# Kernel optimization log

Hardware: AMD Instinct MI355X
Metric: run time of the kernel (lower is better)

## Reference

```python
import jax, jax.numpy as jnp
import numpy as np

TOP_K = 2
NUM_EXPERTS = 8

def setup_inputs() -> dict:
    key = jax.random.key(0)
    k_x, k_r, k_g, k_u, k_d = jax.random.split(key, 5)
    B, L, D, H, E = 1, 2048, 1024, 2048, NUM_EXPERTS
    scale = 0.02  # keep router logits / activations in a sane range
    return {
        "x": jax.random.normal(k_x, (B, L, D), dtype=jnp.float32),
        "router_w": jax.random.normal(k_r, (D, E), dtype=jnp.float32) * scale,
        "gate_w": jax.random.normal(k_g, (E, D, H), dtype=jnp.float32) * scale,
        "up_w": jax.random.normal(k_u, (E, D, H), dtype=jnp.float32) * scale,
        "down_w": jax.random.normal(k_d, (E, H, D), dtype=jnp.float32) * scale,
    }

def reference(x, router_w, gate_w, up_w, down_w):
    # x: (B, L, D)
    B, L, D = x.shape
    T = B * L
    E = router_w.shape[1]
    xf = x.reshape(T, D)

    # --- router: top-k softmax over selected logits (Mixtral-style) ---
    logits = xf @ router_w                      # (T, E)
    top_vals, top_idx = jax.lax.top_k(logits, TOP_K)  # (T, K)
    top_w = jax.nn.softmax(top_vals, axis=-1)   # (T, K)

    # combine weights scattered to dense (T, E); zeros for unrouted experts
    combine = jnp.zeros((T, E), dtype=x.dtype).at[
        jnp.arange(T)[:, None], top_idx
    ].add(top_w)

    # --- experts: SwiGLU, computed per expert, zero-weight tokens masked by combine ---
    gate = jnp.einsum('td,edh->eth', xf, gate_w)   # (E, T, H)
    up = jnp.einsum('td,edh->eth', xf, up_w)       # (E, T, H)
    hidden = jax.nn.silu(gate) * up                # (E, T, H)
    expert_out = jnp.einsum('eth,ehd->etd', hidden, down_w)  # (E, T, D)

    # --- weighted combine (equivalent to scatter_add over sorted assignments) ---
    y = jnp.einsum('etd,te->td', expert_out, combine)  # (T, D)
    return y.reshape(B, L, D)
```

## Files before the change

kernel.cpp:

```cpp
#include <hip/hip_runtime.h>
#include <hip/hip_bf16.h>
#include <stdint.h>

#define T_TOK 2048
#define DIM   1024
#define HDIM  2048
#define NE    8
#define ROWS_PAD 4224
#define TSLOTS 40

typedef __attribute__((ext_vector_type(8))) short bf16x8;
typedef __attribute__((ext_vector_type(8))) unsigned short u16x8;
typedef __attribute__((ext_vector_type(4))) float f32x4;
typedef __attribute__((ext_vector_type(4))) unsigned int u32x4;

__device__ __forceinline__ unsigned short f2bf(float f) {
    union { __hip_bfloat16 h; unsigned short u; } cv;
    cv.h = __float2bfloat16(f);
    return cv.u;
}
__device__ __forceinline__ unsigned int f2bf2(float lo, float hi) {
    union { __hip_bfloat162 h; unsigned int u; } cv;
    cv.h = __float22bfloat162_rn(make_float2(lo, hi));
    return cv.u;
}
__device__ __forceinline__ float bf2f(unsigned short b) {
    union { unsigned int u; float f; } v; v.u = ((unsigned int)b) << 16;
    return v.f;
}

__device__ __forceinline__ void gload16(const void* g, void* l) {
    __builtin_amdgcn_global_load_lds(
        (const __attribute__((address_space(1))) void*)g,
        (__attribute__((address_space(3))) void*)l, 16, 0, 0);
}

__global__ void router_kernel(const float* __restrict__ x, const float* __restrict__ rw,
                              int* __restrict__ counts, int* __restrict__ top_idx,
                              float* __restrict__ top_w) {
    int wid = (blockIdx.x * blockDim.x + threadIdx.x) >> 6;
    int lane = threadIdx.x & 63;
    if (wid >= T_TOK) return;
    float acc[NE];
#pragma unroll
    for (int e = 0; e < NE; ++e) acc[e] = 0.f;
    const float* xr = x + (size_t)wid * DIM;
    for (int i = lane; i < DIM; i += 64) {
        float xv = xr[i];
        const float* wr = rw + (size_t)i * NE;
#pragma unroll
        for (int e = 0; e < NE; ++e) acc[e] += xv * wr[e];
    }
#pragma unroll
    for (int off = 32; off; off >>= 1) {
#pragma unroll
        for (int e = 0; e < NE; ++e) acc[e] += __shfl_xor(acc[e], off, 64);
    }
    if (lane == 0) {
        float v0 = -1e30f, v1 = -1e30f; int i0 = 0, i1 = 0;
#pragma unroll
        for (int e = 0; e < NE; ++e) {
            float v = acc[e];
            if (v > v0) { v1 = v0; i1 = i0; v0 = v; i0 = e; }
            else if (v > v1) { v1 = v; i1 = e; }
        }
        float e1 = __expf(v1 - v0);
        float s = 1.f + e1;
        top_idx[wid * 2]     = i0;
        top_idx[wid * 2 + 1] = i1;
        top_w[wid * 2]     = 1.f / s;
        top_w[wid * 2 + 1] = e1 / s;
        atomicAdd(&counts[i0], 1);
        atomicAdd(&counts[i1], 1);
    }
}

__global__ void scan_kernel(const int* __restrict__ counts, int* __restrict__ offsets,
                            int* __restrict__ cursors,
                            int* __restrict__ tl_e, int* __restrict__ tl_m) {
    if (threadIdx.x == 0) {
        int run = 0;
        for (int e = 0; e < NE; ++e) { offsets[e] = run; cursors[e] = run; run += counts[e]; }
        int n = 0;
        for (int e = 0; e < NE; ++e) {
            int mt = (counts[e] + 127) >> 7;
            for (int m = 0; m < mt && n < 64; ++m) { tl_e[n] = e; tl_m[n] = m; ++n; }
        }
        for (; n < 64; ++n) tl_e[n] = -1;
    }
}

__global__ void gather_kernel(const float* __restrict__ x, const int* __restrict__ top_idx,
                              const float* __restrict__ top_w, int* __restrict__ cursors,
                              int* __restrict__ row_tok, float* __restrict__ row_w,
                              unsigned short* __restrict__ Abuf) {
    int t = blockIdx.x;
    __shared__ int pos[2];
    if (threadIdx.x < 2) {
        int k = threadIdx.x;
        int e = top_idx[t * 2 + k];
        int p = atomicAdd(&cursors[e], 1);
        pos[k] = p;
        row_tok[p] = t;
        row_w[p] = top_w[t * 2 + k];
    }
    __syncthreads();
    const float4* xr = (const float4*)(x + (size_t)t * DIM);
    float4 v = xr[threadIdx.x];
    unsigned int lo = f2bf2(v.x, v.y), hi = f2bf2(v.z, v.w);
    uint2 b; b.x = lo; b.y = hi;
    uint2* A4 = (uint2*)Abuf;
    A4[(size_t)pos[0] * (DIM / 4) + threadIdx.x] = b;
    A4[(size_t)pos[1] * (DIM / 4) + threadIdx.x] = b;
}

__global__ __launch_bounds__(256, 2)
void gemm1_kernel(const unsigned short* __restrict__ Abuf,
                  const float* __restrict__ gw,
                  const float* __restrict__ uw,
                  unsigned short* __restrict__ Hbuf,
                  const int* __restrict__ offsets, const int* __restrict__ counts,
                  const int* __restrict__ tl_e, const int* __restrict__ tl_m) {
    const int slot = blockIdx.y;
    const int e = tl_e[slot];
    if (e < 0) return;
    const int mtile = tl_m[slot];
    const int cnt = counts[e];
    const int n0 = blockIdx.x * 64;
    const int row0 = offsets[e] + mtile * 128;

    __shared__ __align__(16) unsigned char lds_raw[65536];
    unsigned short* AsB = (unsigned short*)lds_raw;
    unsigned short* BgB = (unsigned short*)(lds_raw + 32768);
    unsigned short* BuB = (unsigned short*)(lds_raw + 49152);
    unsigned short* ex  = (unsigned short*)lds_raw;

    const int tid = threadIdx.x;
    const int lane = tid & 63;
    const int wave = tid >> 6;
    const int wm = wave >> 1;
    const int wu = wave & 1;

    f32x4 acc[4][4];
#pragma unroll
    for (int i = 0; i < 4; ++i)
#pragma unroll
        for (int j = 0; j < 4; ++j) acc[i][j] = (f32x4){0.f, 0.f, 0.f, 0.f};

    const int srow = tid >> 3;
    const int sc0 = tid & 7;
    const unsigned short* Aab = Abuf + (size_t)row0 * DIM;

    auto stageA = [&](int buf, int kt) {
#pragma unroll
        for (int i = 0; i < 4; ++i) {
            int row = i * 32 + srow;
            int csrc = sc0 ^ (row & 7);
            gload16(Aab + (size_t)row * DIM + kt + csrc * 8,
                    AsB + buf * 8192 + (i * 256 + tid) * 8);
        }
    };

    const int bn = tid & 63;
    const int bc0 = tid >> 6;
    const float* Bgb = gw + (size_t)e * DIM * HDIM + n0 + bn;
    const float* Bub = uw + (size_t)e * DIM * HDIM + n0 + bn;

    float bgl[2][8], bul[2][8];
    auto bload = [&](int kt) {
#pragma unroll
        for (int cc = 0; cc < 2; ++cc) {
            int c = bc0 + cc * 4;
            const float* gs = Bgb + (size_t)(kt + c * 8) * HDIM;
            const float* us = Bub + (size_t)(kt + c * 8) * HDIM;
#pragma unroll
            for (int jj = 0; jj < 8; ++jj) {
                bgl[cc][jj] = gs[(size_t)jj * HDIM];
                bul[cc][jj] = us[(size_t)jj * HDIM];
            }
        }
    };
    auto bwrite = [&](int buf) {
#pragma unroll
        for (int cc = 0; cc < 2; ++cc) {
            int c = bc0 + cc * 4;
            int la = bn * 64 + ((c ^ (bn & 7)) * 8);
            u32x4 vg, vu;
#pragma unroll
            for (int p = 0; p < 4; ++p) {
                vg[p] = f2bf2(bgl[cc][2 * p], bgl[cc][2 * p + 1]);
                vu[p] = f2bf2(bul[cc][2 * p], bul[cc][2 * p + 1]);
            }
            *(u32x4*)&BgB[buf * 4096 + la] = vg;
            *(u32x4*)&BuB[buf * 4096 + la] = vu;
        }
    };

    const int rsel = lane & 15;
    const int csrcf = lane >> 4;

    stageA(0, 0);
    bload(0);
    bwrite(0);
    int cur = 0;
    for (int kt = 0; kt < DIM; kt += 64) {
        __syncthreads();
        const bool pre = (kt + 64 < DIM);
        if (pre) { stageA(cur ^ 1, kt + 64); bload(kt + 64); }
        const unsigned short* Ac = AsB + cur * 8192;
        const unsigned short* Bc = (wu ? BuB : BgB) + cur * 4096;
#pragma unroll
        for (int kk = 0; kk < 2; ++kk) {
            bf16x8 af[4], bb[4];
#pragma unroll
            for (int i = 0; i < 4; ++i) {
                int ra = wm * 64 + i * 16 + rsel;
                af[i] = *(const bf16x8*)&Ac[ra * 64 + ((kk * 4 + csrcf) ^ (ra & 7)) * 8];
                int rb = i * 16 + rsel;
                bb[i] = *(const bf16x8*)&Bc[rb * 64 + ((kk * 4 + csrcf) ^ (rb & 7)) * 8];
            }
#pragma unroll
            for (int i = 0; i < 4; ++i)
#pragma unroll
                for (int j = 0; j < 4; ++j)
                    acc[i][j] = __builtin_amdgcn_mfma_f32_16x16x32_bf16(af[i], bb[j], acc[i][j], 0, 0, 0);
        }
        if (pre) bwrite(cur ^ 1);
        cur ^= 1;
    }

    const int c = lane & 15, rbase = (lane >> 4) * 4;
    const int obase = offsets[e];
    __syncthreads();
    if (wu) {
#pragma unroll
        for (int i = 0; i < 4; ++i)
#pragma unroll
            for (int r = 0; r < 4; ++r) {
                int row64 = i * 16 + rbase + r;
#pragma unroll
                for (int j = 0; j < 4; ++j)
                    ex[wm * 4096 + row64 * 64 + j * 16 + c] = f2bf(acc[i][j][r]);
            }
    }
    __syncthreads();
    if (!wu) {
#pragma unroll
        for (int i = 0; i < 4; ++i) {
#pragma unroll
            for (int r = 0; r < 4; ++r) {
                int row64 = i * 16 + rbase + r;
                int lrow = mtile * 128 + wm * 64 + row64;
                if (lrow < cnt) {
                    size_t orow = (size_t)(obase + lrow);
#pragma unroll
                    for (int j = 0; j < 4; ++j) {
                        float g = acc[i][j][r];
                        float u = bf2f(ex[wm * 4096 + row64 * 64 + j * 16 + c]);
                        float h = g * u / (1.f + __expf(-g));
                        Hbuf[orow * HDIM + n0 + j * 16 + c] = f2bf(h);
                    }
                }
            }
        }
    }
}

__global__ __launch_bounds__(256, 2)
void gemm2_kernel(const unsigned short* __restrict__ Hbuf,
                  const float* __restrict__ dw,
                  float* __restrict__ y,
                  const int* __restrict__ offsets, const int* __restrict__ counts,
                  const int* __restrict__ row_tok, const float* __restrict__ row_w,
                  const int* __restrict__ tl_e, const int* __restrict__ tl_m) {
    const int slot = blockIdx.y;
    const int e = tl_e[slot];
    if (e < 0) return;
    const int mtile = tl_m[slot];
    const int kc = blockIdx.z;
    const int cnt = counts[e];
    const int n0 = blockIdx.x * 128;
    const int row0 = offsets[e] + mtile * 128;

    __shared__ unsigned short As[2][128 * 64];
    __shared__ unsigned short Bs[2][128 * 64];

    const int tid = threadIdx.x;
    const int lane = tid & 63;
    const int wave = tid >> 6;
    const int wm = wave >> 1, wn = wave & 1;

    f32x4 acc[4][4];
#pragma unroll
    for (int i = 0; i < 4; ++i)
#pragma unroll
        for (int j = 0; j < 4; ++j) acc[i][j] = (f32x4){0.f, 0.f, 0.f, 0.f};

    const int srow0 = tid >> 3;
    const int sc0 = tid & 7;
    const unsigned short* Aab = Hbuf + (size_t)row0 * HDIM;

    auto stageA = [&](int buf, int kt) {
#pragma unroll
        for (int i = 0; i < 4; ++i) {
            int row = i * 32 + srow0;
            int csrc = sc0 ^ (row & 7);
            gload16(Aab + (size_t)row * HDIM + kt + csrc * 8,
                    &As[buf][(i * 256 + tid) * 8]);
        }
    };

    const int bn = tid & 127;
    const int bc0 = (tid >> 7) * 4;
    const float* Bbb = dw + (size_t)e * HDIM * DIM + n0 + bn;

    float bl[4][8];
    auto bload = [&](int kt) {
#pragma unroll
        for (int cc = 0; cc < 4; ++cc) {
            const float* bs = Bbb + (size_t)(kt + (bc0 + cc) * 8) * DIM;
#pragma unroll
            for (int jj = 0; jj < 8; ++jj)
                bl[cc][jj] = bs[(size_t)jj * DIM];
        }
    };
    auto bwrite = [&](int buf) {
#pragma unroll
        for (int cc = 0; cc < 4; ++cc) {
            int c = bc0 + cc;
            int la = bn * 64 + ((c ^ (bn & 7)) * 8);
            u32x4 v;
#pragma unroll
            for (int p = 0; p < 4; ++p)
                v[p] = f2bf2(bl[cc][2 * p], bl[cc][2 * p + 1]);
            *(u32x4*)&Bs[buf][la] = v;
        }
    };

    const int rsel = lane & 15;
    const int csrcf = lane >> 4;

    const int kbeg = kc * (HDIM / 2);
    const int kend = kbeg + (HDIM / 2);

    stageA(0, kbeg);
    bload(kbeg);
    bwrite(0);
    int cur = 0;
    for (int kt = kbeg; kt < kend; kt += 64) {
        __syncthreads();
        const bool pre = (kt + 64 < kend);
        if (pre) { stageA(cur ^ 1, kt + 64); bload(kt + 64); }
        const unsigned short* Ac = As[cur];
        const unsigned short* Bc = Bs[cur];
#pragma unroll
        for (int kk = 0; kk < 2; ++kk) {
            bf16x8 af[4], bf[4];
#pragma unroll
            for (int i = 0; i < 4; ++i) {
                int ra = wm * 64 + i * 16 + rsel;
                af[i] = *(const bf16x8*)&Ac[ra * 64 + ((kk * 4 + csrcf) ^ (ra & 7)) * 8];
                int rb = wn * 64 + i * 16 + rsel;
                bf[i] = *(const bf16x8*)&Bc[rb * 64 + ((kk * 4 + csrcf) ^ (rb & 7)) * 8];
            }
#pragma unroll
            for (int i = 0; i < 4; ++i)
#pragma unroll
                for (int j = 0; j < 4; ++j)
                    acc[i][j] = __builtin_amdgcn_mfma_f32_16x16x32_bf16(af[i], bf[j], acc[i][j], 0, 0, 0);
        }
        if (pre) bwrite(cur ^ 1);
        cur ^= 1;
    }

    const int c = lane & 15, rbase = (lane >> 4) * 4;
    const int obase = offsets[e];
#pragma unroll
    for (int i = 0; i < 4; ++i) {
#pragma unroll
        for (int r = 0; r < 4; ++r) {
            int lrow = mtile * 128 + wm * 64 + i * 16 + rbase + r;
            if (lrow < cnt) {
                int grow = obase + lrow;
                int tok = row_tok[grow];
                float w = row_w[grow];
#pragma unroll
                for (int j = 0; j < 4; ++j) {
                    atomicAdd(&y[(size_t)tok * DIM + n0 + wn * 64 + j * 16 + c], w * acc[i][j][r]);
                }
            }
        }
    }
}

extern "C" void kernel_launch(void* const* d_in, const int* in_sizes, int n_in,
                              void* d_out, int out_size, void* d_ws, size_t ws_size,
                              hipStream_t stream) {
    const float* x  = (const float*)d_in[0];
    const float* rw = (const float*)d_in[1];
    const float* gw = (const float*)d_in[2];
    const float* uw = (const float*)d_in[3];
    const float* dw = (const float*)d_in[4];
    float* y = (float*)d_out;

    char* ws = (char*)d_ws;
    int*   counts  = (int*)(ws + 0);
    int*   cursors = (int*)(ws + 32);
    int*   offsets = (int*)(ws + 64);
    int*   top_idx = (int*)(ws + 128);
    float* top_w   = (float*)(ws + 128 + 16384);
    int*   row_tok = (int*)(ws + 128 + 32768);
    float* row_w   = (float*)(ws + 128 + 32768 + 16896);
    int*   tl_e    = (int*)(ws + 128 + 32768 + 2 * 16896);
    int*   tl_m    = (int*)(ws + 128 + 32768 + 2 * 16896 + 256);
    size_t off = 128 + 32768 + 2 * 16896 + 512;
    off = (off + 255) & ~(size_t)255;
    unsigned short* Abuf = (unsigned short*)(ws + off); off += (size_t)ROWS_PAD * DIM * 2;
    unsigned short* Hbuf = (unsigned short*)(ws + off); off += (size_t)ROWS_PAD * HDIM * 2;
    if (ws_size < off) return;

    hipMemsetAsync(counts, 0, 32, stream);
    hipMemsetAsync(d_out, 0, (size_t)out_size * 4, stream);

    router_kernel<<<T_TOK / 4, 256, 0, stream>>>(x, rw, counts, top_idx, top_w);
    scan_kernel<<<1, 64, 0, stream>>>(counts, offsets, cursors, tl_e, tl_m);
    gather_kernel<<<T_TOK, 256, 0, stream>>>(x, top_idx, top_w, cursors, row_tok, row_w, Abuf);

    gemm1_kernel<<<dim3(HDIM / 64, TSLOTS), 256, 0, stream>>>(Abuf, gw, uw, Hbuf,
                                                              offsets, counts, tl_e, tl_m);
    gemm2_kernel<<<dim3(DIM / 128, TSLOTS, 2), 256, 0, stream>>>(Hbuf, dw, y, offsets, counts,
                                                                 row_tok, row_w, tl_e, tl_m);
}
```

Before: 246.3 us.

## Split fused gate/up GEMM into separate launches with standalone SiLU kernel

The fused gate+up GEMM, which computed both projections per block and combined them through LDS, is split into a grid dimension z=2. Each block now computes only gate or only up on a 128x64 tile, with fewer accumulators and less LDS, and the launch bound is raised to 3 blocks per CU. The SwiGLU combine moves to a separate elementwise kernel that reads the bf16 gate and up buffers and writes H. This aims for more parallelism and occupancy, but it stages A twice, adds an extra kernel launch and roughly 34MB of additional intermediate traffic. The SiLU pass also covers all rows regardless of valid counts.

New measurement: 257.6 us. 4.6% more time.

```diff
diff --git a/kernel.cpp b/kernel.cpp
--- a/kernel.cpp
+++ b/kernel.cpp
@@ -107,20 +107,20 @@
     __syncthreads();
     const float4* xr = (const float4*)(x + (size_t)t * DIM);
     float4 v = xr[threadIdx.x];
-    unsigned int lo = f2bf2(v.x, v.y), hi = f2bf2(v.z, v.w);
-    uint2 b; b.x = lo; b.y = hi;
+    uint2 b; b.x = f2bf2(v.x, v.y); b.y = f2bf2(v.z, v.w);
     uint2* A4 = (uint2*)Abuf;
     A4[(size_t)pos[0] * (DIM / 4) + threadIdx.x] = b;
     A4[(size_t)pos[1] * (DIM / 4) + threadIdx.x] = b;
 }
 
-__global__ __launch_bounds__(256, 2)
-void gemm1_kernel(const unsigned short* __restrict__ Abuf,
-                  const float* __restrict__ gw,
-                  const float* __restrict__ uw,
-                  unsigned short* __restrict__ Hbuf,
-                  const int* __restrict__ offsets, const int* __restrict__ counts,
-                  const int* __restrict__ tl_e, const int* __restrict__ tl_m) {
+__global__ __launch_bounds__(256, 3)
+void gemm1s_kernel(const unsigned short* __restrict__ Abuf,
+                   const float* __restrict__ gw,
+                   const float* __restrict__ uw,
+                   unsigned short* __restrict__ Hg,
+                   unsigned short* __restrict__ Hu,
+                   const int* __restrict__ offsets, const int* __restrict__ counts,
+                   const int* __restrict__ tl_e, const int* __restrict__ tl_m) {
     const int slot = blockIdx.y;
     const int e = tl_e[slot];
     if (e < 0) return;
@@ -128,24 +128,23 @@
     const int cnt = counts[e];
     const int n0 = blockIdx.x * 64;
     const int row0 = offsets[e] + mtile * 128;
-
-    __shared__ __align__(16) unsigned char lds_raw[65536];
-    unsigned short* AsB = (unsigned short*)lds_raw;
-    unsigned short* BgB = (unsigned short*)(lds_raw + 32768);
-    unsigned short* BuB = (unsigned short*)(lds_raw + 49152);
-    unsigned short* ex  = (unsigned short*)lds_raw;
+    const float* W = blockIdx.z ? uw : gw;
+    unsigned short* Hx = blockIdx.z ? Hu : Hg;
+
+    __shared__ unsigned short AsB[2][128 * 64];
+    __shared__ unsigned short Bb[2][64 * 64];
 
     const int tid = threadIdx.x;
     const int lane = tid & 63;
     const int wave = tid >> 6;
     const int wm = wave >> 1;
-    const int wu = wave & 1;
-
-    f32x4 acc[4][4];
+    const int wn = wave & 1;
+
+    f32x4 acc[4][2];
 #pragma unroll
     for (int i = 0; i < 4; ++i)
 #pragma unroll
-        for (int j = 0; j < 4; ++j) acc[i][j] = (f32x4){0.f, 0.f, 0.f, 0.f};
+        for (int j = 0; j < 2; ++j) acc[i][j] = (f32x4){0.f, 0.f, 0.f, 0.f};
 
     const int srow = tid >> 3;
     const int sc0 = tid & 7;
@@ -157,27 +156,23 @@
             int row = i * 32 + srow;
             int csrc = sc0 ^ (row & 7);
             gload16(Aab + (size_t)row * DIM + kt + csrc * 8,
-                    AsB + buf * 8192 + (i * 256 + tid) * 8);
+                    &AsB[buf][(i * 256 + tid) * 8]);
         }
     };
 
     const int bn = tid & 63;
     const int bc0 = tid >> 6;
-    const float* Bgb = gw + (size_t)e * DIM * HDIM + n0 + bn;
-    const float* Bub = uw + (size_t)e * DIM * HDIM + n0 + bn;
-
-    float bgl[2][8], bul[2][8];
+    const float* Bgb = W + (size_t)e * DIM * HDIM + n0 + bn;
+
+    float bl[2][8];
     auto bload = [&](int kt) {
 #pragma unroll
         for (int cc = 0; cc < 2; ++cc) {
             int c = bc0 + cc * 4;
             const float* gs = Bgb + (size_t)(kt + c * 8) * HDIM;
-            const float* us = Bub + (size_t)(kt + c * 8) * HDIM;
-#pragma unroll
-            for (int jj = 0; jj < 8; ++jj) {
-                bgl[cc][jj] = gs[(size_t)jj * HDIM];
-                bul[cc][jj] = us[(size_t)jj * HDIM];
-            }
+#pragma unroll
+            for (int jj = 0; jj < 8; ++jj)
+                bl[cc][jj] = gs[(size_t)jj * HDIM];
         }
     };
     auto bwrite = [&](int buf) {
@@ -185,14 +180,11 @@
         for (int cc = 0; cc < 2; ++cc) {
             int c = bc0 + cc * 4;
             int la = bn * 64 + ((c ^ (bn & 7)) * 8);
-            u32x4 vg, vu;
-#pragma unroll
-            for (int p = 0; p < 4; ++p) {
-                vg[p] = f2bf2(bgl[cc][2 * p], bgl[cc][2 * p + 1]);
-                vu[p] = f2bf2(bul[cc][2 * p], bul[cc][2 * p + 1]);
-            }
-            *(u32x4*)&BgB[buf * 4096 + la] = vg;
-            *(u32x4*)&BuB[buf * 4096 + la] = vu;
+            u32x4 v;
+#pragma unroll
+            for (int p = 0; p < 4; ++p)
+                v[p] = f2bf2(bl[cc][2 * p], bl[cc][2 * p + 1]);
+            *(u32x4*)&Bb[buf][la] = v;
         }
     };
 
@@ -207,22 +199,25 @@
         __syncthreads();
         const bool pre = (kt + 64 < DIM);
         if (pre) { stageA(cur ^ 1, kt + 64); bload(kt + 64); }
-        const unsigned short* Ac = AsB + cur * 8192;
-        const unsigned short* Bc = (wu ? BuB : BgB) + cur * 4096;
+        const unsigned short* Ac = AsB[cur];
+        const unsigned short* Bc = Bb[cur];
 #pragma unroll
         for (int kk = 0; kk < 2; ++kk) {
-            bf16x8 af[4], bb[4];
+            bf16x8 af[4], bb[2];
 #pragma unroll
             for (int i = 0; i < 4; ++i) {
                 int ra = wm * 64 + i * 16 + rsel;
                 af[i] = *(const bf16x8*)&Ac[ra * 64 + ((kk * 4 + csrcf) ^ (ra & 7)) * 8];
-                int rb = i * 16 + rsel;
-                bb[i] = *(const bf16x8*)&Bc[rb * 64 + ((kk * 4 + csrcf) ^ (rb & 7)) * 8];
             }
 #pragma unroll
+            for (int j = 0; j < 2; ++j) {
+                int rb = wn * 32 + j * 16 + rsel;
+                bb[j] = *(const bf16x8*)&Bc[rb * 64 + ((kk * 4 + csrcf) ^ (rb & 7)) * 8];
+            }
+#pragma unroll
             for (int i = 0; i < 4; ++i)
 #pragma unroll
-                for (int j = 0; j < 4; ++j)
+                for (int j = 0; j < 2; ++j)
                     acc[i][j] = __builtin_amdgcn_mfma_f32_16x16x32_bf16(af[i], bb[j], acc[i][j], 0, 0, 0);
         }
         if (pre) bwrite(cur ^ 1);
@@ -231,39 +226,34 @@
 
     const int c = lane & 15, rbase = (lane >> 4) * 4;
     const int obase = offsets[e];
-    __syncthreads();
-    if (wu) {
-#pragma unroll
-        for (int i = 0; i < 4; ++i)
-#pragma unroll
-            for (int r = 0; r < 4; ++r) {
-                int row64 = i * 16 + rbase + r;
-#pragma unroll
-                for (int j = 0; j < 4; ++j)
-                    ex[wm * 4096 + row64 * 64 + j * 16 + c] = f2bf(acc[i][j][r]);
+#pragma unroll
+    for (int i = 0; i < 4; ++i) {
+#pragma unroll
+        for (int r = 0; r < 4; ++r) {
+            int lrow = mtile * 128 + wm * 64 + i * 16 + rbase + r;
+            if (lrow < cnt) {
+                size_t orow = (size_t)(obase + lrow);
+#pragma unroll
+                for (int j = 0; j < 2; ++j)
+                    Hx[orow * HDIM + n0 + wn * 32 + j * 16 + c] = f2bf(acc[i][j][r]);
             }
-    }
-    __syncthreads();
-    if (!wu) {
-#pragma unroll
-        for (int i = 0; i < 4; ++i) {
-#pragma unroll
-            for (int r = 0; r < 4; ++r) {
-                int row64 = i * 16 + rbase + r;
-                int lrow = mtile * 128 + wm * 64 + row64;
-                if (lrow < cnt) {
-                    size_t orow = (size_t)(obase + lrow);
-#pragma unroll
-                    for (int j = 0; j < 4; ++j) {
-                        float g = acc[i][j][r];
-                        float u = bf2f(ex[wm * 4096 + row64 * 64 + j * 16 + c]);
-                        float h = g * u / (1.f + __expf(-g));
-                        Hbuf[orow * HDIM + n0 + j * 16 + c] = f2bf(h);
-                    }
-                }
-            }
-        }
-    }
+        }
+    }
+}
+
+__global__ void silu_kernel(const unsigned short* __restrict__ Hg,
+                            const unsigned short* __restrict__ Hu,
+                            unsigned short* __restrict__ Hbuf) {
+    size_t idx = ((size_t)blockIdx.x * 256 + threadIdx.x) * 8;
+    u16x8 g8 = *(const u16x8*)&Hg[idx];
+    u16x8 u8 = *(const u16x8*)&Hu[idx];
+    u16x8 h8;
+#pragma unroll
+    for (int k = 0; k < 8; ++k) {
+        float g = bf2f(g8[k]), u = bf2f(u8[k]);
+        h8[k] = f2bf(g * u / (1.f + __expf(-g)));
+    }
+    *(u16x8*)&Hbuf[idx] = h8;
 }
 
 __global__ __launch_bounds__(256, 2)
@@ -417,6 +407,8 @@
     off = (off + 255) & ~(size_t)255;
     unsigned short* Abuf = (unsigned short*)(ws + off); off += (size_t)ROWS_PAD * DIM * 2;
     unsigned short* Hbuf = (unsigned short*)(ws + off); off += (size_t)ROWS_PAD * HDIM * 2;
+    unsigned short* Hg   = (unsigned short*)(ws + off); off += (size_t)ROWS_PAD * HDIM * 2;
+    unsigned short* Hu   = (unsigned short*)(ws + off); off += (size_t)ROWS_PAD * HDIM * 2;
     if (ws_size < off) return;
 
     hipMemsetAsync(counts, 0, 32, stream);
@@ -426,8 +418,9 @@
     scan_kernel<<<1, 64, 0, stream>>>(counts, offsets, cursors, tl_e, tl_m);
     gather_kernel<<<T_TOK, 256, 0, stream>>>(x, top_idx, top_w, cursors, row_tok, row_w, Abuf);
 
-    gemm1_kernel<<<dim3(HDIM / 64, TSLOTS), 256, 0, stream>>>(Abuf, gw, uw, Hbuf,
-                                                              offsets, counts, tl_e, tl_m);
+    gemm1s_kernel<<<dim3(HDIM / 64, TSLOTS, 2), 256, 0, stream>>>(Abuf, gw, uw, Hg, Hu,
+                                                                  offsets, counts, tl_e, tl_m);
+    silu_kernel<<<(T_TOK * 2 * HDIM) / (256 * 8), 256, 0, stream>>>(Hg, Hu, Hbuf);
     gemm2_kernel<<<dim3(DIM / 128, TSLOTS, 2), 256, 0, stream>>>(Hbuf, dw, y, offsets, counts,
                                                                  row_tok, row_w, tl_e, tl_m);
 }
```
